# Kernel tuning notes

Measured on AMD Instinct MI355X. Metric: run time of the kernel, lower is better.

Reference implementation:

```python
import jax, jax.numpy as jnp
import numpy as np

WS = 32  # window size hardcoded in the original module

def _dwconv7(x, w, b):
    # x: (B,C,H,W), w: (C,1,7,7) depthwise
    y = jax.lax.conv_general_dilated(
        x, w, window_strides=(1, 1), padding='SAME',
        dimension_numbers=('NCHW', 'OIHW', 'NCHW'),
        feature_group_count=x.shape[1])
    return y + b[None, :, None, None]


def setup_inputs() -> dict:
    key = jax.random.key(0)
    ks = jax.random.split(key, 9)
    B, C, H, W = 4, 64, 128, 128
    x = jax.random.normal(ks[0], (B, C, H, W), dtype=jnp.float32)
    s = 0.05
    conv1_w = jax.random.normal(ks[1], (C, 1, 7, 7), dtype=jnp.float32) * s
    conv1_b = jax.random.normal(ks[2], (C,), dtype=jnp.float32) * s
    conv2_w = jax.random.normal(ks[3], (C, C), dtype=jnp.float32) * s
    conv2_b = jax.random.normal(ks[4], (C,), dtype=jnp.float32) * s
    conv3_w = jax.random.normal(ks[5], (C, C), dtype=jnp.float32) * s
    conv3_b = jax.random.normal(ks[6], (C,), dtype=jnp.float32) * s
    conv4_w = jax.random.normal(ks[7], (C, C), dtype=jnp.float32) * s
    conv4_b = jax.random.normal(ks[8], (C,), dtype=jnp.float32) * s
    return {'x': x, 'conv1_w': conv1_w, 'conv1_b': conv1_b,
            'conv2_w': conv2_w, 'conv2_b': conv2_b,
            'conv3_w': conv3_w, 'conv3_b': conv3_b,
            'conv4_w': conv4_w, 'conv4_b': conv4_b}


def reference(x, conv1_w, conv1_b, conv2_w, conv2_b, conv3_w, conv3_b, conv4_w, conv4_b):
    B, C, H, W = x.shape
    scale = jnp.asarray(C, x.dtype) ** -0.5
    h = _dwconv7(x, conv1_w, conv1_b)
    # window partition: (B,C,H,W) -> (N, C, WS*WS) with N = B*(H/WS)*(W/WS)
    hw = h.reshape(B, C, H // WS, WS, W // WS, WS)
    hw = hw.transpose(0, 2, 4, 1, 3, 5).reshape(-1, C, WS * WS)  # (N,C,P)
    # 1x1 convs as channel matmuls
    q = jnp.einsum('oc,ncp->nop', conv2_w, hw) + conv2_b[None, :, None]  # (N,C,P)
    k = jnp.einsum('oc,ncp->nop', conv3_w, hw) + conv3_b[None, :, None]  # (N,C,P)
    # att = k^T @ q * scale, softmax over dim 1 (first spatial axis)
    att = jnp.einsum('ncp,ncq->npq', k, q) * scale  # (N,P,P)
    att = jax.nn.softmax(att, axis=1)
    out = jnp.einsum('ncp,npq->ncq', hw, att)  # (N,C,P)
    out = jnp.einsum('oc,ncq->noq', conv4_w, out) + conv4_b[None, :, None]
    # un-partition back to (B,C,H,W)
    out = out.reshape(B, H // WS, W // WS, C, WS, WS)
    out = out.transpose(0, 3, 1, 4, 2, 5).reshape(B, C, H, W)
    return out
```

## Files before the change

### kernel.cpp

```cpp
#include <hip/hip_runtime.h>

typedef unsigned int  u32;
typedef unsigned short u16;
typedef short s16x8 __attribute__((ext_vector_type(8)));
typedef float f32x16 __attribute__((ext_vector_type(16)));

#define BB   4
#define CC   64
#define HH   128
#define WW   128
#define NWIN 64
#define PP   1024

__device__ __forceinline__ u16 f2bf(float f) {
  u32 x = __float_as_uint(f);
  return (u16)((x + 0x7fffu + ((x >> 16) & 1u)) >> 16);
}
__device__ __forceinline__ u32 pk2(float a, float b) {
  return (u32)f2bf(a) | ((u32)f2bf(b) << 16);
}

__global__ __launch_bounds__(256)
void dwconv_kernel(const float* __restrict__ x, const float* __restrict__ w,
                   const float* __restrict__ bias, float* __restrict__ hw,
                   u16* __restrict__ vb, float* __restrict__ vsum) {
  int blk = blockIdx.x;
  int n = blk >> 6, c = blk & 63;
  int b = n >> 4, wy = (n >> 2) & 3, wx = n & 3;
  int y0 = wy * 32 - 3, x0 = wx * 32 - 3;
  __shared__ float patch[38][40];
  __shared__ float wf[49];
  __shared__ float wsum[4];
  int tid = threadIdx.x;
  if (tid < 49) wf[tid] = w[c * 49 + tid];
  const float* xp = x + (size_t)(b * CC + c) * HH * WW;
  for (int i = tid; i < 38 * 38; i += 256) {
    int py = i / 38, px = i - py * 38;
    int gy = y0 + py, gx = x0 + px;
    float v = 0.f;
    if (gy >= 0 && gy < HH && gx >= 0 && gx < WW) v = xp[gy * WW + gx];
    patch[py][px] = v;
  }
  __syncthreads();
  float bv = bias[c];
  int yy = tid >> 3;
  int xg = (tid & 7) << 2;
  float o0_ = bv, o1_ = bv, o2_ = bv, o3_ = bv;
  #pragma unroll
  for (int dy = 0; dy < 7; ++dy) {
    const float* pr = &patch[yy + dy][xg];
    float4 ra = *(const float4*)pr;
    float4 rb = *(const float4*)(pr + 4);
    float4 rc = *(const float4*)(pr + 8);
    float rv[12] = {ra.x, ra.y, ra.z, ra.w, rb.x, rb.y, rb.z, rb.w,
                    rc.x, rc.y, rc.z, rc.w};
    #pragma unroll
    for (int dx = 0; dx < 7; ++dx) {
      float wgt = wf[dy * 7 + dx];
      o0_ = fmaf(rv[dx],     wgt, o0_);
      o1_ = fmaf(rv[dx + 1], wgt, o1_);
      o2_ = fmaf(rv[dx + 2], wgt, o2_);
      o3_ = fmaf(rv[dx + 3], wgt, o3_);
    }
  }
  size_t obase = (size_t)(n * CC + c) * PP + yy * 32 + xg;
  *(float4*)(hw + obase) = make_float4(o0_, o1_, o2_, o3_);
  *(uint2*)(vb + obase) = make_uint2(pk2(o0_, o1_), pk2(o2_, o3_));
  float psum = (o0_ + o1_) + (o2_ + o3_);
  #pragma unroll
  for (int off = 1; off < 64; off <<= 1) psum += __shfl_xor(psum, off);
  if ((tid & 63) == 0) wsum[tid >> 6] = psum;
  __syncthreads();
  if (tid == 0) vsum[blk] = (wsum[0] + wsum[1]) + (wsum[2] + wsum[3]);
}

__global__ __launch_bounds__(256)
void qk_kernel(const float* __restrict__ hw,
               const float* __restrict__ w2, const float* __restrict__ b2,
               const float* __restrict__ w3, const float* __restrict__ b3,
               u16* __restrict__ qT, u16* __restrict__ kT) {
  int n = blockIdx.x >> 4;
  int chunk = blockIdx.x & 15;
  int tid = threadIdx.x;
  int lane = tid & 63, wvi = tid >> 6;
  int l31 = lane & 31, hi = lane >> 5;
  int phalf = wvi & 1, ochalf = wvi >> 1;
  int p0 = (chunk << 6) + (phalf << 5);
  int oc0 = ochalf << 5;

  union FU { u32 u[4]; s16x8 v; };

  s16x8 bq[4], bk[4];
  {
    const float* w2r = w2 + (oc0 + l31) * 64 + (hi << 3);
    const float* w3r = w3 + (oc0 + l31) * 64 + (hi << 3);
    #pragma unroll
    for (int kst = 0; kst < 4; ++kst) {
      float4 a = *(const float4*)(w2r + kst * 16);
      float4 b = *(const float4*)(w2r + kst * 16 + 4);
      FU f;
      f.u[0] = pk2(a.x * 0.125f, a.y * 0.125f);
      f.u[1] = pk2(a.z * 0.125f, a.w * 0.125f);
      f.u[2] = pk2(b.x * 0.125f, b.y * 0.125f);
      f.u[3] = pk2(b.z * 0.125f, b.w * 0.125f);
      bq[kst] = f.v;
      float4 c = *(const float4*)(w3r + kst * 16);
      float4 d = *(const float4*)(w3r + kst * 16 + 4);
      f.u[0] = pk2(c.x, c.y); f.u[1] = pk2(c.z, c.w);
      f.u[2] = pk2(d.x, d.y); f.u[3] = pk2(d.z, d.w);
      bk[kst] = f.v;
    }
  }

  f32x16 accq, acck;
  #pragma unroll
  for (int j = 0; j < 16; ++j) { accq[j] = 0.f; acck[j] = 0.f; }

  const float* hbase = hw + ((size_t)n << 16) + (size_t)(hi << 3) * PP
                       + p0 + l31;
  #pragma unroll
  for (int kst = 0; kst < 4; ++kst) {
    const float* hp = hbase + (size_t)(kst * 16) * PP;
    float h[8];
    #pragma unroll
    for (int e = 0; e < 8; ++e) h[e] = hp[e * PP];
    FU fh, fl;
    #pragma unroll
    for (int t = 0; t < 4; ++t) {
      u32 ph;
      asm("v_cvt_pk_bf16_f32 %0, %1, %2"
          : "=v"(ph) : "v"(h[2 * t]), "v"(h[2 * t + 1]));
      fh.u[t] = ph;
      float r0 = h[2 * t]     - __uint_as_float(ph << 16);
      float r1 = h[2 * t + 1] - __uint_as_float(ph & 0xffff0000u);
      u32 pl;
      asm("v_cvt_pk_bf16_f32 %0, %1, %2" : "=v"(pl) : "v"(r0), "v"(r1));
      fl.u[t] = pl;
    }
    accq = __builtin_amdgcn_mfma_f32_32x32x16_bf16(fh.v, bq[kst], accq, 0, 0, 0);
    accq = __builtin_amdgcn_mfma_f32_32x32x16_bf16(fl.v, bq[kst], accq, 0, 0, 0);
    acck = __builtin_amdgcn_mfma_f32_32x32x16_bf16(fh.v, bk[kst], acck, 0, 0, 0);
    acck = __builtin_amdgcn_mfma_f32_32x32x16_bf16(fl.v, bk[kst], acck, 0, 0, 0);
  }

  float biasq = b2[oc0 + l31] * 0.125f;
  float biask = b3[oc0 + l31];
  u16* qrow = qT + (((size_t)n << 10) + p0) * 64 + oc0 + l31;
  u16* krow = kT + (((size_t)n << 10) + p0) * 64 + oc0 + l31;
  #pragma unroll
  for (int r = 0; r < 16; ++r) {
    int pr = (r & 3) + ((r >> 2) << 3) + (hi << 2);
    qrow[pr * 64] = f2bf(accq[r] + biasq);
    krow[pr * 64] = f2bf(acck[r] + biask);
  }
}

__global__ __launch_bounds__(256)
void attn_kernel(const u16* __restrict__ qT, const u16* __restrict__ kT,
                 const u16* __restrict__ vB, const float* __restrict__ vsum,
                 const float* __restrict__ w4, const float* __restrict__ b4,
                 float* __restrict__ outp) {
  int bid = blockIdx.x;
  int w = (bid & 7) * 64 + (bid >> 3);
  int n = w >> 3, qb = w & 7;
  int tid = threadIdx.x;

  __shared__ __align__(16) unsigned char QsB[16384];
  __shared__ __align__(16) unsigned char KsB[8192];
  __shared__ __align__(16) unsigned char VsB[8192];
  __shared__ float l_inv[4][32];

  const size_t nbase = (size_t)n << 16;

  {
    const u16* qg = qT + nbase + ((size_t)qb << 13);
    for (int i = tid; i < 1024; i += 256) {
      int row = i >> 3, c8 = i & 7;
      uint4 v = *(const uint4*)(qg + row * 64 + c8 * 8);
      *(uint4*)(QsB + row * 128 + ((c8 * 16) ^ ((row & 7) << 4))) = v;
    }
  }

  int lane = tid & 63, wv = tid >> 6;
  int l31 = lane & 31, hi = lane >> 5;
  int sz = (lane & 7) << 4;
  int hi16 = hi << 4;

  f32x16 o0, o1;
  #pragma unroll
  for (int j = 0; j < 16; ++j) { o0[j] = 0.f; o1[j] = 0.f; }
  float lsum = 0.f;

  const u16* kg = kT + nbase;
  const u16* vg = vB + nbase;
  int qrow = (wv << 5) + l31;

  for (int pt = 0; pt < 16; ++pt) {
    __syncthreads();
    int p0 = pt << 6;
    for (int i = tid; i < 512; i += 256) {
      int row = i >> 3, c8 = i & 7;
      int dst = row * 128 + ((c8 * 16) ^ ((row & 7) << 4));
      uint4 kv4 = *(const uint4*)(kg + (size_t)(p0 + row) * 64 + c8 * 8);
      *(uint4*)(KsB + dst) = kv4;
      uint4 vv4 = *(const uint4*)(vg + (size_t)row * 1024 + p0 + c8 * 8);
      *(uint4*)(VsB + dst) = vv4;
    }
    __syncthreads();

    f32x16 s0, s1;
    #pragma unroll
    for (int j = 0; j < 16; ++j) { s0[j] = 0.f; s1[j] = 0.f; }
    #pragma unroll
    for (int kc = 0; kc < 4; ++kc) {
      int cb = kc * 32 + hi16;
      s16x8 b  = *(const s16x8*)(QsB + qrow * 128 + (cb ^ sz));
      s16x8 a0 = *(const s16x8*)(KsB + l31 * 128 + (cb ^ sz));
      s16x8 a1 = *(const s16x8*)(KsB + (32 + l31) * 128 + (cb ^ sz));
      s0 = __builtin_amdgcn_mfma_f32_32x32x16_bf16(a0, b, s0, 0, 0, 0);
      s1 = __builtin_amdgcn_mfma_f32_32x32x16_bf16(a1, b, s1, 0, 0, 0);
    }

    #pragma unroll
    for (int j = 0; j < 16; ++j) {
      float e = __expf(s0[j]); lsum += e; s0[j] = e - 1.0f;
    }
    #pragma unroll
    for (int j = 0; j < 16; ++j) {
      float e = __expf(s1[j]); lsum += e; s1[j] = e - 1.0f;
    }

    u32 t0,t1,t2,t3,t4,t5,t6,t7, u0,u1,u2,u3,u4,u5,u6,u7;
#define CVT(d, a, b) asm("v_cvt_pk_bf16_f32 %0, %1, %2" : "=v"(d) : "v"(a), "v"(b))
#define SWP(a, b)    asm("v_permlane32_swap_b32 %0, %1" : "+v"(a), "+v"(b))
    CVT(t0, s0[0],  s0[1]);  CVT(t1, s0[2],  s0[3]);
    CVT(t2, s0[4],  s0[5]);  CVT(t3, s0[6],  s0[7]);
    CVT(t4, s0[8],  s0[9]);  CVT(t5, s0[10], s0[11]);
    CVT(t6, s0[12], s0[13]); CVT(t7, s0[14], s0[15]);
    SWP(t0, t2); SWP(t1, t3); SWP(t4, t6); SWP(t5, t7);
    CVT(u0, s1[0],  s1[1]);  CVT(u1, s1[2],  s1[3]);
    CVT(u2, s1[4],  s1[5]);  CVT(u3, s1[6],  s1[7]);
    CVT(u4, s1[8],  s1[9]);  CVT(u5, s1[10], s1[11]);
    CVT(u6, s1[12], s1[13]); CVT(u7, s1[14], s1[15]);
    SWP(u0, u2); SWP(u1, u3); SWP(u4, u6); SWP(u5, u7);
#undef CVT
#undef SWP
    union FU { u32 u[4]; s16x8 v; };
    FU fA; fA.u[0]=t0; fA.u[1]=t1; fA.u[2]=t2; fA.u[3]=t3;
    FU fB; fB.u[0]=t4; fB.u[1]=t5; fB.u[2]=t6; fB.u[3]=t7;
    FU fC; fC.u[0]=u0; fC.u[1]=u1; fC.u[2]=u2; fC.u[3]=u3;
    FU fD; fD.u[0]=u4; fD.u[1]=u5; fD.u[2]=u6; fD.u[3]=u7;

#define PV_STEP(frag, pb) do { \
      s16x8 bv0 = *(const s16x8*)(VsB + l31 * 128 + ((pb) ^ sz)); \
      s16x8 bv1 = *(const s16x8*)(VsB + (32 + l31) * 128 + ((pb) ^ sz)); \
      o0 = __builtin_amdgcn_mfma_f32_32x32x16_bf16(frag, bv0, o0, 0, 0, 0); \
      o1 = __builtin_amdgcn_mfma_f32_32x32x16_bf16(frag, bv1, o1, 0, 0, 0); \
    } while (0)
    PV_STEP(fA.v, 0 + hi16);
    PV_STEP(fB.v, 32 + hi16);
    PV_STEP(fC.v, 64 + hi16);
    PV_STEP(fD.v, 96 + hi16);
#undef PV_STEP
  }

  lsum += __shfl_xor(lsum, 32);
  if (hi == 0) l_inv[wv][l31] = 1.0f / lsum;

  float vs0 = vsum[(n << 6) + l31];
  float vs1 = vsum[(n << 6) + 32 + l31];
  int g0 = l31 >> 3, g1 = (32 + l31) >> 3;
  int bi = (l31 & 7) << 1;
  #pragma unroll
  for (int r = 0; r < 16; ++r) {
    int qr = (r & 3) + ((r >> 2) << 3) + (hi << 2);
    int row = (wv << 5) + qr;
    float li = l_inv[wv][qr];
    int rs = (row & 7) << 4;
    *(u16*)(QsB + row * 128 + ((g0 << 4) ^ rs) + bi) = f2bf((vs0 + o0[r]) * li);
    *(u16*)(QsB + row * 128 + ((g1 << 4) ^ rs) + bi) = f2bf((vs1 + o1[r]) * li);
  }

  union FU2 { u32 u[4]; s16x8 v; };
  int orow = (wv << 5) + l31;
  int osw = (orow & 7) << 4;
  s16x8 bf[4];
  #pragma unroll
  for (int kst = 0; kst < 4; ++kst)
    bf[kst] = *(const s16x8*)(QsB + orow * 128 + ((((kst << 1) + hi) << 4) ^ osw));

  f32x16 d2a, d2b;
  #pragma unroll
  for (int j = 0; j < 16; ++j) { d2a[j] = 0.f; d2b[j] = 0.f; }
  {
    const float* w4r = w4 + l31 * 64 + (hi << 3);
    #pragma unroll
    for (int kst = 0; kst < 4; ++kst) {
      float4 a = *(const float4*)(w4r + kst * 16);
      float4 b = *(const float4*)(w4r + kst * 16 + 4);
      FU2 f;
      f.u[0] = pk2(a.x, a.y); f.u[1] = pk2(a.z, a.w);
      f.u[2] = pk2(b.x, b.y); f.u[3] = pk2(b.z, b.w);
      d2a = __builtin_amdgcn_mfma_f32_32x32x16_bf16(f.v, bf[kst], d2a, 0, 0, 0);
    }
    const float* w4r2 = w4 + (32 + l31) * 64 + (hi << 3);
    #pragma unroll
    for (int kst = 0; kst < 4; ++kst) {
      float4 a = *(const float4*)(w4r2 + kst * 16);
      float4 b = *(const float4*)(w4r2 + kst * 16 + 4);
      FU2 f;
      f.u[0] = pk2(a.x, a.y); f.u[1] = pk2(a.z, a.w);
      f.u[2] = pk2(b.x, b.y); f.u[3] = pk2(b.z, b.w);
      d2b = __builtin_amdgcn_mfma_f32_32x32x16_bf16(f.v, bf[kst], d2b, 0, 0, 0);
    }
  }

  int b_ = n >> 4, wy = (n >> 2) & 3, wx = n & 3;
  int y = wy * 32 + (qb << 2) + wv;
  int x = wx * 32 + l31;
  float* obase = outp + ((size_t)b_ * CC * HH + y) * WW + x;
  #pragma unroll
  for (int r = 0; r < 16; ++r) {
    int ocr = (r & 3) + ((r >> 2) << 3) + (hi << 2);
    obase[(size_t)ocr * HH * WW]        = d2a[r] + b4[ocr];
    obase[(size_t)(32 + ocr) * HH * WW] = d2b[r] + b4[32 + ocr];
  }
}

extern "C" void kernel_launch(void* const* d_in, const int* in_sizes, int n_in,
                              void* d_out, int out_size, void* d_ws, size_t ws_size,
                              hipStream_t stream) {
  const float* x  = (const float*)d_in[0];
  const float* w1 = (const float*)d_in[1];
  const float* b1 = (const float*)d_in[2];
  const float* w2 = (const float*)d_in[3];
  const float* b2 = (const float*)d_in[4];
  const float* w3 = (const float*)d_in[5];
  const float* b3 = (const float*)d_in[6];
  const float* w4 = (const float*)d_in[7];
  const float* b4 = (const float*)d_in[8];
  float* outp = (float*)d_out;

  char* wsb = (char*)d_ws;
  float* hw   = (float*)wsb;
  u16*   qT   = (u16*)(wsb + (16u << 20));
  u16*   kT   = (u16*)(wsb + (24u << 20));
  u16*   vb   = (u16*)(wsb + (32u << 20));
  float* vsum = (float*)(wsb + (40u << 20));

  dwconv_kernel<<<NWIN * CC, 256, 0, stream>>>(x, w1, b1, hw, vb, vsum);
  qk_kernel   <<<NWIN * 16, 256, 0, stream>>>(hw, w2, b2, w3, b3, qT, kT);
  attn_kernel <<<NWIN * 8,  256, 0, stream>>>(qT, kT, vb, vsum, w4, b4, outp);
}
```

Baseline: 151.5 us.

## Load Q/K/V MFMA fragments directly from global memory, dropping LDS staging

```diff
diff --git a/kernel.cpp b/kernel.cpp
--- a/kernel.cpp
+++ b/kernel.cpp
@@ -165,26 +165,21 @@
   int n = w >> 3, qb = w & 7;
   int tid = threadIdx.x;
 
-  __shared__ __align__(16) unsigned char QsB[16384];
-  __shared__ __align__(16) unsigned char KsB[8192];
-  __shared__ __align__(16) unsigned char VsB[8192];
+  __shared__ __align__(16) unsigned char Osm[16384];
   __shared__ float l_inv[4][32];
-
-  const size_t nbase = (size_t)n << 16;
-
-  {
-    const u16* qg = qT + nbase + ((size_t)qb << 13);
-    for (int i = tid; i < 1024; i += 256) {
-      int row = i >> 3, c8 = i & 7;
-      uint4 v = *(const uint4*)(qg + row * 64 + c8 * 8);
-      *(uint4*)(QsB + row * 128 + ((c8 * 16) ^ ((row & 7) << 4))) = v;
-    }
-  }
 
   int lane = tid & 63, wv = tid >> 6;
   int l31 = lane & 31, hi = lane >> 5;
-  int sz = (lane & 7) << 4;
-  int hi16 = hi << 4;
+
+  const size_t nbase = (size_t)n << 16;
+
+  s16x8 qf[4];
+  {
+    const u16* qp = qT + nbase
+                    + (size_t)((qb << 7) + (wv << 5) + l31) * 64 + (hi << 3);
+    #pragma unroll
+    for (int kc = 0; kc < 4; ++kc) qf[kc] = *(const s16x8*)(qp + kc * 16);
+  }
 
   f32x16 o0, o1;
   #pragma unroll
@@ -193,32 +188,25 @@
 
   const u16* kg = kT + nbase;
   const u16* vg = vB + nbase;
-  int qrow = (wv << 5) + l31;
 
   for (int pt = 0; pt < 16; ++pt) {
-    __syncthreads();
     int p0 = pt << 6;
-    for (int i = tid; i < 512; i += 256) {
-      int row = i >> 3, c8 = i & 7;
-      int dst = row * 128 + ((c8 * 16) ^ ((row & 7) << 4));
-      uint4 kv4 = *(const uint4*)(kg + (size_t)(p0 + row) * 64 + c8 * 8);
-      *(uint4*)(KsB + dst) = kv4;
-      uint4 vv4 = *(const uint4*)(vg + (size_t)row * 1024 + p0 + c8 * 8);
-      *(uint4*)(VsB + dst) = vv4;
-    }
-    __syncthreads();
+
+    const u16* k0p = kg + (size_t)(p0 + l31) * 64 + (hi << 3);
+    s16x8 kf0[4], kf1[4];
+    #pragma unroll
+    for (int kc = 0; kc < 4; ++kc) {
+      kf0[kc] = *(const s16x8*)(k0p + kc * 16);
+      kf1[kc] = *(const s16x8*)(k0p + 2048 + kc * 16);
+    }
 
     f32x16 s0, s1;
     #pragma unroll
     for (int j = 0; j < 16; ++j) { s0[j] = 0.f; s1[j] = 0.f; }
     #pragma unroll
     for (int kc = 0; kc < 4; ++kc) {
-      int cb = kc * 32 + hi16;
-      s16x8 b  = *(const s16x8*)(QsB + qrow * 128 + (cb ^ sz));
-      s16x8 a0 = *(const s16x8*)(KsB + l31 * 128 + (cb ^ sz));
-      s16x8 a1 = *(const s16x8*)(KsB + (32 + l31) * 128 + (cb ^ sz));
-      s0 = __builtin_amdgcn_mfma_f32_32x32x16_bf16(a0, b, s0, 0, 0, 0);
-      s1 = __builtin_amdgcn_mfma_f32_32x32x16_bf16(a1, b, s1, 0, 0, 0);
+      s0 = __builtin_amdgcn_mfma_f32_32x32x16_bf16(kf0[kc], qf[kc], s0, 0, 0, 0);
+      s1 = __builtin_amdgcn_mfma_f32_32x32x16_bf16(kf1[kc], qf[kc], s1, 0, 0, 0);
     }
 
     #pragma unroll
@@ -251,16 +239,17 @@
     FU fC; fC.u[0]=u0; fC.u[1]=u1; fC.u[2]=u2; fC.u[3]=u3;
     FU fD; fD.u[0]=u4; fD.u[1]=u5; fD.u[2]=u6; fD.u[3]=u7;
 
-#define PV_STEP(frag, pb) do { \
-      s16x8 bv0 = *(const s16x8*)(VsB + l31 * 128 + ((pb) ^ sz)); \
-      s16x8 bv1 = *(const s16x8*)(VsB + (32 + l31) * 128 + ((pb) ^ sz)); \
+    const u16* v0p = vg + (size_t)l31 * 1024 + p0 + (hi << 3);
+#define PV_STEP(frag, ps) do { \
+      s16x8 bv0 = *(const s16x8*)(v0p + (ps) * 16); \
+      s16x8 bv1 = *(const s16x8*)(v0p + 32768 + (ps) * 16); \
       o0 = __builtin_amdgcn_mfma_f32_32x32x16_bf16(frag, bv0, o0, 0, 0, 0); \
       o1 = __builtin_amdgcn_mfma_f32_32x32x16_bf16(frag, bv1, o1, 0, 0, 0); \
     } while (0)
-    PV_STEP(fA.v, 0 + hi16);
-    PV_STEP(fB.v, 32 + hi16);
-    PV_STEP(fC.v, 64 + hi16);
-    PV_STEP(fD.v, 96 + hi16);
+    PV_STEP(fA.v, 0);
+    PV_STEP(fB.v, 1);
+    PV_STEP(fC.v, 2);
+    PV_STEP(fD.v, 3);
 #undef PV_STEP
   }
 
@@ -277,8 +266,8 @@
     int row = (wv << 5) + qr;
     float li = l_inv[wv][qr];
     int rs = (row & 7) << 4;
-    *(u16*)(QsB + row * 128 + ((g0 << 4) ^ rs) + bi) = f2bf((vs0 + o0[r]) * li);
-    *(u16*)(QsB + row * 128 + ((g1 << 4) ^ rs) + bi) = f2bf((vs1 + o1[r]) * li);
+    *(u16*)(Osm + row * 128 + ((g0 << 4) ^ rs) + bi) = f2bf((vs0 + o0[r]) * li);
+    *(u16*)(Osm + row * 128 + ((g1 << 4) ^ rs) + bi) = f2bf((vs1 + o1[r]) * li);
   }
 
   union FU2 { u32 u[4]; s16x8 v; };
@@ -287,7 +276,7 @@
   s16x8 bf[4];
   #pragma unroll
   for (int kst = 0; kst < 4; ++kst)
-    bf[kst] = *(const s16x8*)(QsB + orow * 128 + ((((kst << 1) + hi) << 4) ^ osw));
+    bf[kst] = *(const s16x8*)(Osm + orow * 128 + ((((kst << 1) + hi) << 4) ^ osw));
 
   f32x16 d2a, d2b;
   #pragma unroll
```

Result: slower. 182.6 us (+20.5%).
